# Performance work log

Measured on AMD Instinct MI355X. Metric: run time of the kernel, lower is better.

## Reference

```python
import jax, jax.numpy as jnp
import numpy as np

LAMBDA_COORD = 5.0
LAMBDA_NOOBJ = 0.5
B, N, F = 2048, 64, 19  # batch, nb_pred, 2 + n_classes


def _greedy_scan(Permut, v, h, D2, mask, n):
    # One greedy-assignment phase: n sequential argmax/one-hot steps.
    def step(carry, _):
        Permut, v, h, D2 = carry
        D2 = D2 * v[:, :, None] * h[:, None, :]
        A = jax.nn.one_hot(jnp.argmax(D2, axis=-1), n, dtype=D2.dtype)          # row-wise best col
        Bm = v[:, :, None] * A * D2
        C = jnp.swapaxes(jax.nn.one_hot(jnp.argmax(Bm, axis=-2), n, dtype=D2.dtype), -1, -2)  # col-wise best row
        E = v[:, :, None] * A * C
        Permut = Permut + E
        v = (1.0 - Permut.sum(-1)) * mask
        h = 1.0 - Permut.sum(-2)
        return (Permut, v, h, D2), None
    (Permut, v, h, D2), _ = jax.lax.scan(step, (Permut, v, h, D2), None, length=n)
    return Permut, v, h, D2


def _permute_ypred(y_true, y_pred):
    alpha = y_true[:, :, 0]                      # [B, N] in {0,1}
    x = y_true[:, :, 1]
    p = y_pred[:, :, 1]
    n = x.shape[-1]
    D1 = 1.0 - jnp.abs(x[:, :, None] - p[:, None, :])   # [B, N, N] similarity

    # Phase 1: match ground-truth positives (rows with alpha=1).
    Permut0 = jnp.zeros_like(D1)
    v0 = alpha
    h0 = jnp.ones_like(alpha)
    D2_0 = v0[:, :, None] * D1
    Permut, v, h, _ = _greedy_scan(Permut0, v0, h0, D2_0, alpha, n)

    # Phase 2: match remaining rows (alpha=0) to remaining predictions.
    neg = 1.0 - alpha
    D2_1 = neg[:, :, None] * D1 * h[:, None, :]
    Permut, _, _, _ = _greedy_scan(Permut, neg, h, D2_1, neg, n)

    permutation = jnp.argmax(Permut, axis=-1)            # [B, N]
    idx = jnp.broadcast_to(permutation[:, :, None], y_pred.shape)
    return jnp.take_along_axis(y_pred, idx, axis=1)


def setup_inputs() -> dict:
    key = jax.random.key(0)
    k1, k2, k3 = jax.random.split(key, 3)
    y_true = jax.random.uniform(k1, (B, N, F), dtype=jnp.float32)
    alpha = (jax.random.uniform(k3, (B, N)) < 0.3).astype(jnp.float32)
    y_true = y_true.at[:, :, 0].set(alpha)
    y_pred = jax.random.uniform(k2, (B, N, F), dtype=jnp.float32)
    return {"y_true": y_true, "y_pred": y_pred}


def reference(y_true, y_pred):
    y_pred = _permute_ypred(y_true, y_pred)
    a = y_true[:, :, 0]
    loss = jnp.sum(
        a * LAMBDA_COORD * jnp.square(y_true[:, :, 1] - y_pred[:, :, 1])
        + a * jnp.square(a - y_pred[:, :, 0])
        + (1.0 - a) * LAMBDA_NOOBJ * jnp.square(a - y_pred[:, :, 0])
        + a * jnp.sum(jnp.square(y_true[:, :, 2:] - y_pred[:, :, 2:]), axis=-1)
    )
    return loss
```

## Files before the change

### kernel.cpp

```cpp
#include <hip/hip_runtime.h>
#include <stdint.h>


#define NN 64
#define NF 19
#define NW (NN * NF)
#define NW4 (NW / 4)
#define WPB 4

#define WSYNC() asm volatile("s_waitcnt lgkmcnt(0)" ::: "memory")

__global__ __launch_bounds__(WPB * 64) void spotting_loss_kernel(
    const float* __restrict__ yt, const float* __restrict__ yp,
    float* __restrict__ ws, int nbatch)
{
  const int wid = threadIdx.x >> 6;
  const int i   = threadIdx.x & 63;
  const int b   = blockIdx.x * WPB + wid;
  if (b >= nbatch) return;

  const float4* __restrict__ yt4 = (const float4*)(yt + (size_t)b * NW);
  const float4* __restrict__ yp4 = (const float4*)(yp + (size_t)b * NW);

  __shared__ float4 yts4[WPB][NW4];
  __shared__ float4 yps4[WPB][NW4];
  __shared__ unsigned long long key_lds[WPB][NN];
  const float* __restrict__ yts = (const float*)&yts4[wid][0];
  const float* __restrict__ yps = (const float*)&yps4[wid][0];
  unsigned long long* __restrict__ key_sh = &key_lds[wid][0];

#pragma unroll
  for (int k = 0; k < 5; ++k) {
    const int idx = i + 64 * k;
    if (idx < NW4) {
      yts4[wid][idx] = yt4[idx];
      yps4[wid][idx] = yp4[idx];
    }
  }
  WSYNC();

  const float alpha = yts[i * NF + 0];
  const float x     = yts[i * NF + 1];

  float D1r[NN];
#pragma unroll
  for (int j = 0; j < NN; ++j) {
    D1r[j] = 1.0f - fabsf(x - yps[j * NF + 1]);
  }

  unsigned long long hbits = ~0ull;
  int   perm  = 0;
  int   jmax  = 0;
  float best  = 0.0f;

  for (int phase = 0; phase < 2; ++phase) {
    bool vlive  = (phase == 0) ? (alpha > 0.5f) : (alpha < 0.5f);
    bool rescan = vlive;

    for (int it = 0; it < NN; ++it) {
      if (__ballot(vlive) == 0ull) break;

      if (rescan) {
        const unsigned hlo = (unsigned)hbits;
        const unsigned hhi = (unsigned)(hbits >> 32);
        best = -1.0f; jmax = 0;
#pragma unroll
        for (int j = 0; j < NN; ++j) {
          const unsigned bit = (j < 32) ? ((hlo >> j) & 1u)
                                        : ((hhi >> (j - 32)) & 1u);
          const unsigned msk = 0u - bit;
          const float t = __uint_as_float(__float_as_uint(D1r[j]) & msk);
          if (t > best) { best = t; jmax = j; }
        }
        rescan = false;
      }

      key_sh[i] = 63ull;
      WSYNC();

      if (vlive && best > 0.0f) {
        const unsigned long long key =
            (((unsigned long long)__float_as_uint(best)) << 6) |
            (unsigned long long)(63 - i);
        atomicMax(&key_sh[jmax], key);
      }
      WSYNC();

      const unsigned long long kc = key_sh[i];
      const bool colkill = (kc >> 6) != 0ull;
      const unsigned long long killed = __ballot(colkill);

      if (vlive) {
        const unsigned long long kw = key_sh[jmax];
        const int winner = 63 - (int)(kw & 63ull);
        if (winner == i) {
          perm = jmax;
          vlive = false;
        } else if ((killed >> jmax) & 1ull) {
          rescan = true;
        }
      }
      hbits &= ~killed;
      WSYNC();
    }
  }

  const float* __restrict__ ypr = yps + perm * NF;
  const float* __restrict__ ytr = yts + i * NF;
  const float a  = alpha;
  const float p0 = ypr[0];
  const float p1 = ypr[1];
  const float dx = x - p1;
  const float da = a - p0;
  float s2 = 0.0f;
#pragma unroll
  for (int f = 2; f < NF; ++f) {
    const float d = ytr[f] - ypr[f];
    s2 += d * d;
  }
  float l = a * 5.0f * (dx * dx)
          + a * (da * da)
          + (1.0f - a) * 0.5f * (da * da)
          + a * s2;

#pragma unroll
  for (int off = 32; off > 0; off >>= 1) l += __shfl_down(l, off);
  if (i == 0) ws[b] = l;
}

__global__ __launch_bounds__(256) void reduce_ws_kernel(
    const float* __restrict__ ws, float* __restrict__ out, int nb)
{
  const int t = threadIdx.x;
  float s = 0.0f;
  for (int j = t; j < nb; j += 256) s += ws[j];
  __shared__ float part[4];
#pragma unroll
  for (int off = 32; off > 0; off >>= 1) s += __shfl_down(s, off);
  if ((t & 63) == 0) part[t >> 6] = s;
  __syncthreads();
  if (t == 0) out[0] = part[0] + part[1] + part[2] + part[3];
}

extern "C" void kernel_launch(void* const* d_in, const int* in_sizes, int n_in,
                              void* d_out, int out_size, void* d_ws, size_t ws_size,
                              hipStream_t stream) {
  const float* yt = (const float*)d_in[0];
  const float* yp = (const float*)d_in[1];
  float* out = (float*)d_out;
  float* ws  = (float*)d_ws;
  const int B = in_sizes[0] / (NN * NF);
  const int nblk = (B + WPB - 1) / WPB;

  if (out_size > 1) {
    hipMemsetAsync(out, 0, sizeof(float) * (size_t)out_size, stream);
  }
  spotting_loss_kernel<<<nblk, WPB * 64, 0, stream>>>(yt, yp, ws, B);
  reduce_ws_kernel<<<1, 256, 0, stream>>>(ws, out, B);
}
```

Baseline: 113.5 us.

## Process two batches per wave and drop per-iteration key reset and barrier

Each wavefront now handles two batch items in sequence and keeps a running loss sum, which halves the number of partial sums the reduction kernel reads. The LDS auction keys are reset once per batch instead of every greedy iteration, because claimed columns keep their keys and are already masked out of later searches. This removes one LDS store and one wait from each iteration. The cost is half as many concurrent waves on a latency-bound kernel, which leaves less room to hide LDS and ballot latency.

```diff
diff --git a/kernel.cpp b/kernel.cpp
--- a/kernel.cpp
+++ b/kernel.cpp
@@ -7,6 +7,8 @@
 #define NW (NN * NF)
 #define NW4 (NW / 4)
 #define WPB 4
+#define KB  2
+typedef unsigned long long u64;
 
 #define WSYNC() asm volatile("s_waitcnt lgkmcnt(0)" ::: "memory")
 
@@ -16,116 +18,121 @@
 {
   const int wid = threadIdx.x >> 6;
   const int i   = threadIdx.x & 63;
-  const int b   = blockIdx.x * WPB + wid;
-  if (b >= nbatch) return;
-
-  const float4* __restrict__ yt4 = (const float4*)(yt + (size_t)b * NW);
-  const float4* __restrict__ yp4 = (const float4*)(yp + (size_t)b * NW);
+  const int g   = blockIdx.x * WPB + wid;
 
   __shared__ float4 yts4[WPB][NW4];
   __shared__ float4 yps4[WPB][NW4];
-  __shared__ unsigned long long key_lds[WPB][NN];
+  __shared__ u64 key_lds[WPB][NN];
   const float* __restrict__ yts = (const float*)&yts4[wid][0];
   const float* __restrict__ yps = (const float*)&yps4[wid][0];
-  unsigned long long* __restrict__ key_sh = &key_lds[wid][0];
+  u64* __restrict__ key_sh = &key_lds[wid][0];
+
+  float lsum = 0.0f;
+
+#pragma unroll 1
+  for (int q = 0; q < KB; ++q) {
+    const int b = g * KB + q;
+    if (b >= nbatch) break;
+
+    const float4* __restrict__ yt4 = (const float4*)(yt + (size_t)b * NW);
+    const float4* __restrict__ yp4 = (const float4*)(yp + (size_t)b * NW);
 
 #pragma unroll
-  for (int k = 0; k < 5; ++k) {
-    const int idx = i + 64 * k;
-    if (idx < NW4) {
-      yts4[wid][idx] = yt4[idx];
-      yps4[wid][idx] = yp4[idx];
+    for (int k = 0; k < 5; ++k) {
+      const int idx = i + 64 * k;
+      if (idx < NW4) {
+        yts4[wid][idx] = yt4[idx];
+        yps4[wid][idx] = yp4[idx];
+      }
     }
-  }
-  WSYNC();
+    key_sh[i] = 63ull;
+    WSYNC();
 
-  const float alpha = yts[i * NF + 0];
-  const float x     = yts[i * NF + 1];
+    const float alpha = yts[i * NF + 0];
+    const float x     = yts[i * NF + 1];
 
-  float D1r[NN];
+    float D1r[NN];
 #pragma unroll
-  for (int j = 0; j < NN; ++j) {
-    D1r[j] = 1.0f - fabsf(x - yps[j * NF + 1]);
-  }
+    for (int j = 0; j < NN; ++j) {
+      D1r[j] = 1.0f - fabsf(x - yps[j * NF + 1]);
+    }
 
-  unsigned long long hbits = ~0ull;
-  int   perm  = 0;
-  int   jmax  = 0;
-  float best  = 0.0f;
+    u64   hbits = ~0ull;
+    int   perm  = 0;
+    int   jmax  = 0;
+    float best  = 0.0f;
 
-  for (int phase = 0; phase < 2; ++phase) {
-    bool vlive  = (phase == 0) ? (alpha > 0.5f) : (alpha < 0.5f);
-    bool rescan = vlive;
+    for (int phase = 0; phase < 2; ++phase) {
+      bool vlive  = (phase == 0) ? (alpha > 0.5f) : (alpha < 0.5f);
+      bool rescan = vlive;
 
-    for (int it = 0; it < NN; ++it) {
-      if (__ballot(vlive) == 0ull) break;
+      for (int it = 0; it < NN; ++it) {
+        if (__ballot(vlive) == 0ull) break;
 
-      if (rescan) {
-        const unsigned hlo = (unsigned)hbits;
-        const unsigned hhi = (unsigned)(hbits >> 32);
-        best = -1.0f; jmax = 0;
+        if (rescan) {
+          const unsigned hlo = (unsigned)hbits;
+          const unsigned hhi = (unsigned)(hbits >> 32);
+          best = -1.0f; jmax = 0;
 #pragma unroll
-        for (int j = 0; j < NN; ++j) {
-          const unsigned bit = (j < 32) ? ((hlo >> j) & 1u)
-                                        : ((hhi >> (j - 32)) & 1u);
-          const unsigned msk = 0u - bit;
-          const float t = __uint_as_float(__float_as_uint(D1r[j]) & msk);
-          if (t > best) { best = t; jmax = j; }
+          for (int j = 0; j < NN; ++j) {
+            const unsigned bit = (j < 32) ? ((hlo >> j) & 1u)
+                                          : ((hhi >> (j - 32)) & 1u);
+            const unsigned msk = 0u - bit;
+            const float t = __uint_as_float(__float_as_uint(D1r[j]) & msk);
+            if (t > best) { best = t; jmax = j; }
+          }
+          rescan = false;
         }
-        rescan = false;
+
+        if (vlive && best > 0.0f) {
+          const u64 key = (((u64)__float_as_uint(best)) << 6) |
+                          (u64)(63 - i);
+          atomicMax(&key_sh[jmax], key);
+        }
+        WSYNC();
+
+        const u64 kc = key_sh[i];
+        const u64 kw = key_sh[jmax];
+        WSYNC();
+
+        const bool colkill = (kc >> 6) != 0ull;
+        const u64 killed = __ballot(colkill);
+
+        if (vlive) {
+          const int winner = 63 - (int)(kw & 63ull);
+          if (winner == i) {
+            perm  = jmax;
+            vlive = false;
+          } else if ((killed >> jmax) & 1ull) {
+            rescan = true;
+          }
+        }
+        hbits &= ~killed;
       }
+    }
 
-      key_sh[i] = 63ull;
-      WSYNC();
-
-      if (vlive && best > 0.0f) {
-        const unsigned long long key =
-            (((unsigned long long)__float_as_uint(best)) << 6) |
-            (unsigned long long)(63 - i);
-        atomicMax(&key_sh[jmax], key);
-      }
-      WSYNC();
-
-      const unsigned long long kc = key_sh[i];
-      const bool colkill = (kc >> 6) != 0ull;
-      const unsigned long long killed = __ballot(colkill);
-
-      if (vlive) {
-        const unsigned long long kw = key_sh[jmax];
-        const int winner = 63 - (int)(kw & 63ull);
-        if (winner == i) {
-          perm = jmax;
-          vlive = false;
-        } else if ((killed >> jmax) & 1ull) {
-          rescan = true;
-        }
-      }
-      hbits &= ~killed;
-      WSYNC();
+    const float* __restrict__ ypr = yps + perm * NF;
+    const float* __restrict__ ytr = yts + i * NF;
+    const float a  = alpha;
+    const float p0 = ypr[0];
+    const float p1 = ypr[1];
+    const float dx = x - p1;
+    const float da = a - p0;
+    float s2 = 0.0f;
+#pragma unroll
+    for (int f = 2; f < NF; ++f) {
+      const float d = ytr[f] - ypr[f];
+      s2 += d * d;
     }
-  }
-
-  const float* __restrict__ ypr = yps + perm * NF;
-  const float* __restrict__ ytr = yts + i * NF;
-  const float a  = alpha;
-  const float p0 = ypr[0];
-  const float p1 = ypr[1];
-  const float dx = x - p1;
-  const float da = a - p0;
-  float s2 = 0.0f;
-#pragma unroll
-  for (int f = 2; f < NF; ++f) {
-    const float d = ytr[f] - ypr[f];
-    s2 += d * d;
-  }
-  float l = a * 5.0f * (dx * dx)
+    lsum += a * 5.0f * (dx * dx)
           + a * (da * da)
           + (1.0f - a) * 0.5f * (da * da)
           + a * s2;
+  }
 
 #pragma unroll
-  for (int off = 32; off > 0; off >>= 1) l += __shfl_down(l, off);
-  if (i == 0) ws[b] = l;
+  for (int off = 32; off > 0; off >>= 1) lsum += __shfl_down(lsum, off);
+  if (i == 0) ws[g] = lsum;
 }
 
 __global__ __launch_bounds__(256) void reduce_ws_kernel(
@@ -150,11 +157,12 @@
   float* out = (float*)d_out;
   float* ws  = (float*)d_ws;
   const int B = in_sizes[0] / (NN * NF);
-  const int nblk = (B + WPB - 1) / WPB;
+  const int nwaves = (B + KB - 1) / KB;
+  const int nblk = (nwaves + WPB - 1) / WPB;
 
   if (out_size > 1) {
     hipMemsetAsync(out, 0, sizeof(float) * (size_t)out_size, stream);
   }
   spotting_loss_kernel<<<nblk, WPB * 64, 0, stream>>>(yt, yp, ws, B);
-  reduce_ws_kernel<<<1, 256, 0, stream>>>(ws, out, B);
+  reduce_ws_kernel<<<1, 256, 0, stream>>>(ws, out, nwaves);
 }
```

New measurement: 137.0 us. +20.7%, slower.
